# Kernel tuning notes

Measured on AMD Instinct MI355X. Metric: run time of the kernel, lower is better.

## Reference

```python
import jax, jax.numpy as jnp
import numpy as np
from jax.scipy.special import logsumexp

N = 36
N_ITERS = 20
TAU = 0.05
B = 512


def _xavier(key, out_f, in_f):
    std = float(np.sqrt(2.0 / (in_f + out_f)))
    return jax.random.normal(key, (out_f, in_f), dtype=jnp.float32) * std


def setup_inputs() -> dict:
    key = jax.random.key(0)
    ks = jax.random.split(key, 8)
    seq = jax.random.normal(ks[0], (B, N, 3076), dtype=jnp.float32)
    return {
        "seq": seq,
        "W1_txt_w": _xavier(ks[1], 128, 512), "W1_txt_b": jnp.zeros((128,), jnp.float32),
        "W1_vis_w": _xavier(ks[2], 512, 2048), "W1_vis_b": jnp.zeros((512,), jnp.float32),
        "W2_vis_w": _xavier(ks[3], 128, 512), "W2_vis_b": jnp.zeros((128,), jnp.float32),
        "W1_sen_w": _xavier(ks[4], 128, 512), "W1_sen_b": jnp.zeros((128,), jnp.float32),
        "W_fc_pos_w": _xavier(ks[5], 256, 388), "W_fc_pos_b": jnp.zeros((256,), jnp.float32),
        "W_fc_w": _xavier(ks[6], N, 256), "W_fc_b": jnp.zeros((N,), jnp.float32),
    }


def _linear(x, w, b):
    return x @ w.T + b


def _sinkhorn(x):
    # Faithful to the torch code: x = exp(x/tau); then iterative logsumexp
    # subtraction over rows/cols; finally exp(x).
    x = jnp.exp(x / TAU)

    def body(i, x):
        x = x - logsumexp(x, axis=-1, keepdims=True)
        x = x - logsumexp(x, axis=-2, keepdims=True)
        return x

    x = jax.lax.fori_loop(0, N_ITERS, body, x)
    return jnp.exp(x)


def reference(seq, W1_txt_w, W1_txt_b, W1_vis_w, W1_vis_b, W2_vis_w, W2_vis_b,
              W1_sen_w, W1_sen_b, W_fc_pos_w, W_fc_pos_b, W_fc_w, W_fc_b):
    x_txt = seq[:, :, :512]
    x_vis = seq[:, :, 512:2560]
    x_pos = seq[:, :, 2560:2564]
    x_sen = seq[:, :, 2564:]
    x_txt = jax.nn.relu(_linear(x_txt, W1_txt_w, W1_txt_b))
    x_vis = jax.nn.relu(_linear(x_vis, W1_vis_w, W1_vis_b))
    x_vis = jax.nn.relu(_linear(x_vis, W2_vis_w, W2_vis_b))
    x_sen = jax.nn.relu(_linear(x_sen, W1_sen_w, W1_sen_b))
    x_pos = jax.nn.relu(x_pos)
    x = jnp.concatenate((x_txt, x_vis, x_pos, x_sen), axis=-1)  # [B, N, 388]
    x = jax.nn.relu(_linear(x, W_fc_pos_w, W_fc_pos_b))
    x = jnp.tanh(_linear(x, W_fc_w, W_fc_b))  # [B, N, N]
    return _sinkhorn(x)
```

## Files before the change

kernel.cpp:

```cpp
#include <hip/hip_runtime.h>
#include <cstddef>
#include <cstdint>
#include <cmath>

#define TAU_INV 20.0f
#define NMAT 36
#define BATCH 512
#define MROWS 18432
#define MHALF 9216

typedef unsigned short us16;
typedef __attribute__((ext_vector_type(8))) short s16x8;
typedef __attribute__((ext_vector_type(4))) float f32x4;

__device__ inline us16 f2bf(float x) {
    uint32_t u = __float_as_uint(x);
    u += 0x7fff + ((u >> 16) & 1);
    return (us16)(u >> 16);
}
__device__ inline float bf2f(us16 h) {
    return __uint_as_float(((uint32_t)h) << 16);
}
__device__ inline void split3(float v, us16& h, us16& m, us16& l) {
    h = f2bf(v);
    float r1 = v - bf2f(h);
    m = f2bf(r1);
    l = f2bf(r1 - bf2f(m));
}

__device__ inline uint32_t cvtpk(float lo, float hi) {
    uint32_t d;
    asm("v_cvt_pk_bf16_f32 %0, %1, %2" : "=v"(d) : "v"(lo), "v"(hi));
    return d;
}
__device__ inline void split2pk(const float4& v, uint2& h, uint2& m) {
    uint32_t h0 = cvtpk(v.x, v.y), h1 = cvtpk(v.z, v.w);
    float a0 = v.x - __uint_as_float(h0 << 16);
    float a1 = v.y - __uint_as_float(h0 & 0xffff0000u);
    float a2 = v.z - __uint_as_float(h1 << 16);
    float a3 = v.w - __uint_as_float(h1 & 0xffff0000u);
    uint32_t m0 = cvtpk(a0, a1), m1 = cvtpk(a2, a3);
    h = make_uint2(h0, h1); m = make_uint2(m0, m1);
}

__device__ inline void dma16(const void* g, void* l) {
    __builtin_amdgcn_global_load_lds(
        (const __attribute__((address_space(1))) void*)g,
        (__attribute__((address_space(3))) void*)l, 16, 0, 0);
}

__device__ inline f32x4 mfma16(s16x8 a, s16x8 b, f32x4 c) {
    return __builtin_amdgcn_mfma_f32_16x16x32_bf16(a, b, c, 0, 0, 0);
}

template<int BM, int BN, int OUT, int MINW>
__global__ __launch_bounds__(256, MINW)
void gemm_split(const float* X, int ldx,
                const us16* Bh, const us16* Bm,
                const float* bias, float* C, int ldc, int nreal, int K,
                const float* X2, const us16* Bh2, const us16* Bm2,
                const float* bias2, float* C2)
{
    constexpr int MT  = BM / 32;
    constexpr int NT  = BN / 32;
    constexpr int NF4 = BM / 32;
    constexpr int LB  = BN / 64;

    if (blockIdx.z) { X = X2; Bh = Bh2; Bm = Bm2; bias = bias2; C = C2; }

    alignas(16) __shared__ us16 lds[(BM + BN) * 64];
    us16* AsH = lds;
    us16* AsM = lds + BM * 32;
    us16* BsH = lds + BM * 64;
    us16* BsM = lds + BM * 64 + BN * 32;

    const int tid  = threadIdx.x;
    const int lane = tid & 63;
    const int wid  = tid >> 6;
    const int bm   = blockIdx.x * BM;
    const int bn   = blockIdx.y * BN;
    const int lm   = lane & 15;
    const int kb   = lane >> 4;
    const int wm   = (wid >> 1) * (BM / 2);
    const int wn   = (wid & 1) * (BN / 2);

    const int arow = tid >> 3;
    const int acol = (tid & 7) * 4;
    const int asw  = ((arow >> 1) & 3) << 3;
    const int fsw  = ((lm >> 1) & 3) << 3;

    f32x4 acc[MT][NT];
#pragma unroll
    for (int i = 0; i < MT; ++i)
#pragma unroll
        for (int j = 0; j < NT; ++j) acc[i][j] = (f32x4){0.f, 0.f, 0.f, 0.f};

    float4 pref[NF4];
#pragma unroll
    for (int i = 0; i < NF4; ++i)
        pref[i] = *(const float4*)(X + (size_t)(bm + i * 32 + arow) * ldx + acol);

    const int bcol = ((lane & 3) ^ ((lane >> 3) & 3)) * 8;

    for (int k0 = 0; k0 < K; k0 += 32) {
        __syncthreads();
#pragma unroll
        for (int q = 0; q < LB; ++q) {
            const int rb = wid * (LB * 16) + q * 16;
            const int gr = bn + rb + (lane >> 2);
            const int gc = k0 + bcol;
            dma16(Bh + (size_t)gr * K + gc, &BsH[rb * 32]);
            dma16(Bm + (size_t)gr * K + gc, &BsM[rb * 32]);
        }
        float4 prefN[NF4];
        if (k0 + 32 < K) {
#pragma unroll
            for (int i = 0; i < NF4; ++i)
                prefN[i] = *(const float4*)(X + (size_t)(bm + i * 32 + arow) * ldx
                                            + (k0 + 32) + acol);
        }
#pragma unroll
        for (int i = 0; i < NF4; ++i) {
            const int r = i * 32 + arow;
            uint2 h, m;
            split2pk(pref[i], h, m);
            *(uint2*)&AsH[r * 32 + (acol ^ asw)] = h;
            *(uint2*)&AsM[r * 32 + (acol ^ asw)] = m;
        }
        if (k0 + 32 < K) {
#pragma unroll
            for (int i = 0; i < NF4; ++i) pref[i] = prefN[i];
        }
        __syncthreads();

        s16x8 ah[MT], am[MT];
#pragma unroll
        for (int mt = 0; mt < MT; ++mt) {
            const int off = (wm + mt * 16 + lm) * 32 + (kb * 8 ^ fsw);
            ah[mt] = *(const s16x8*)&AsH[off];
            am[mt] = *(const s16x8*)&AsM[off];
        }
#pragma unroll
        for (int nt = 0; nt < NT; ++nt) {
            const int off = (wn + nt * 16 + lm) * 32 + (kb * 8 ^ fsw);
            s16x8 bfh = *(const s16x8*)&BsH[off];
            s16x8 bfm = *(const s16x8*)&BsM[off];
#pragma unroll
            for (int mt = 0; mt < MT; ++mt) {
                acc[mt][nt] = mfma16(ah[mt], bfh, acc[mt][nt]);
                acc[mt][nt] = mfma16(ah[mt], bfm, acc[mt][nt]);
                acc[mt][nt] = mfma16(am[mt], bfh, acc[mt][nt]);
                acc[mt][nt] = mfma16(am[mt], bfm, acc[mt][nt]);
            }
        }
    }

    float bv[NT];
#pragma unroll
    for (int nt = 0; nt < NT; ++nt) {
        const int col = bn + wn + nt * 16 + lm;
        bv[nt] = (col < nreal) ? bias[col] : 0.f;
    }
#pragma unroll
    for (int nt = 0; nt < NT; ++nt) {
        const int col = bn + wn + nt * 16 + lm;
#pragma unroll
        for (int mt = 0; mt < MT; ++mt) {
#pragma unroll
            for (int r = 0; r < 4; ++r) {
                const int row = bm + wm + mt * 16 + kb * 4 + r;
                float v = acc[mt][nt][r] + bv[nt];
                if (OUT == 0) {
                    C[(size_t)row * ldc + col] = fmaxf(v, 0.f);
                } else {
                    if (col < nreal)
                        C[(size_t)row * ldc + col] = tanhf(v);
                }
            }
        }
    }
}

#define WOFF_W1T 1048576
#define WOFF_W1S 1114112
#define WOFF_W2V 1179648
#define WOFF_WFP 1245184
#define WOFF_WFC 1351680
#define WTOT     1368064

__global__ void split_weights(const float* __restrict__ w1v, const float* __restrict__ w1t,
                              const float* __restrict__ w1s, const float* __restrict__ w2v,
                              const float* __restrict__ wfp, const float* __restrict__ wfc,
                              us16* __restrict__ hi, us16* __restrict__ mi,
                              us16* __restrict__ lo)
{
    int idx = blockIdx.x * 256 + threadIdx.x;
    if (idx >= WTOT) return;
    const float* src; int N, K, Kp; int local;
    if (idx < WOFF_W1T)      { src = w1v; N = 512; K = 2048; Kp = 2048; local = idx; }
    else if (idx < WOFF_W1S) { src = w1t; N = 128; K = 512;  Kp = 512;  local = idx - WOFF_W1T; }
    else if (idx < WOFF_W2V) { src = w1s; N = 128; K = 512;  Kp = 512;  local = idx - WOFF_W1S; }
    else if (idx < WOFF_WFP) { src = w2v; N = 128; K = 512;  Kp = 512;  local = idx - WOFF_W2V; }
    else if (idx < WOFF_WFC) { src = wfp; N = 256; K = 388;  Kp = 416;  local = idx - WOFF_WFP; }
    else                     { src = wfc; N = 36;  K = 256;  Kp = 256;  local = idx - WOFF_WFC; }
    int n = local / Kp, k = local % Kp;
    float v = (n < N && k < K) ? src[(size_t)n * K + k] : 0.f;
    us16 h, m, l;
    split3(v, h, m, l);
    hi[idx] = h; mi[idx] = m; lo[idx] = l;
}

__global__ void pos_pad(const float* __restrict__ seq, float* __restrict__ cat)
{
    int idx = blockIdx.x * 256 + threadIdx.x;
    if (idx >= MROWS * 32) return;
    int row = idx >> 5, j = idx & 31;
    if (j < 4) {
        float v = seq[(size_t)row * 3076 + 2560 + j];
        cat[(size_t)row * 416 + 256 + j] = fmaxf(v, 0.f);
    } else {
        cat[(size_t)row * 416 + 388 + (j - 4)] = 0.f;
    }
}

__global__ __launch_bounds__(256)
void sinkhorn_kernel(const float* __restrict__ Z, float* __restrict__ out)
{
    __shared__ float A[NMAT][NMAT + 1];
    __shared__ float lse[NMAT];
    const int b = blockIdx.x;
    const int tid = threadIdx.x;
    const float* zb = Z + (size_t)b * NMAT * NMAT;

    for (int idx = tid; idx < NMAT * NMAT; idx += 256)
        A[idx / NMAT][idx % NMAT] = expf(zb[idx] * TAU_INV);
    __syncthreads();

    for (int it = 0; it < 20; ++it) {
        if (tid < NMAT * 4) {
            int r = tid >> 2, g = tid & 3;
            float m = -3.402823466e38f;
            for (int j = g; j < NMAT; j += 4) m = fmaxf(m, A[r][j]);
            m = fmaxf(m, __shfl_xor(m, 2, 4));
            m = fmaxf(m, __shfl_xor(m, 1, 4));
            float s = 0.f;
            for (int j = g; j < NMAT; j += 4) s += expf(A[r][j] - m);
            s += __shfl_xor(s, 2, 4);
            s += __shfl_xor(s, 1, 4);
            if (g == 0) lse[r] = m + logf(s);
        }
        __syncthreads();
        for (int idx = tid; idx < NMAT * NMAT; idx += 256)
            A[idx / NMAT][idx % NMAT] -= lse[idx / NMAT];
        __syncthreads();

        if (tid < NMAT * 4) {
            int c = tid >> 2, g = tid & 3;
            float m = -3.402823466e38f;
            for (int i = g; i < NMAT; i += 4) m = fmaxf(m, A[i][c]);
            m = fmaxf(m, __shfl_xor(m, 2, 4));
            m = fmaxf(m, __shfl_xor(m, 1, 4));
            float s = 0.f;
            for (int i = g; i < NMAT; i += 4) s += expf(A[i][c] - m);
            s += __shfl_xor(s, 2, 4);
            s += __shfl_xor(s, 1, 4);
            if (g == 0) lse[c] = m + logf(s);
        }
        __syncthreads();
        for (int idx = tid; idx < NMAT * NMAT; idx += 256)
            A[idx / NMAT][idx % NMAT] -= lse[idx % NMAT];
        __syncthreads();
    }

    for (int idx = tid; idx < NMAT * NMAT; idx += 256)
        out[(size_t)b * NMAT * NMAT + idx] = expf(A[idx / NMAT][idx % NMAT]);
}

extern "C" void kernel_launch(void* const* d_in, const int* in_sizes, int n_in,
                              void* d_out, int out_size, void* d_ws, size_t ws_size,
                              hipStream_t stream)
{
    const float* seq = (const float*)d_in[0];
    const float* W1t = (const float*)d_in[1];
    const float* b1t = (const float*)d_in[2];
    const float* W1v = (const float*)d_in[3];
    const float* b1v = (const float*)d_in[4];
    const float* W2v = (const float*)d_in[5];
    const float* b2v = (const float*)d_in[6];
    const float* W1s = (const float*)d_in[7];
    const float* b1s = (const float*)d_in[8];
    const float* Wfp = (const float*)d_in[9];
    const float* bfp = (const float*)d_in[10];
    const float* Wfc = (const float*)d_in[11];
    const float* bfc = (const float*)d_in[12];

    float* wsF = (float*)d_ws;
    dim3 blk(256);

    const bool full = ws_size >= (size_t)19156992 * 4;

    if (full) {
        float* vis1buf = wsF;
        float* h256    = wsF;
        float* cat     = wsF + 9437184;
        float* logits  = wsF + 9437184;
        us16*  Whi     = (us16*)(wsF + 17104896);
        us16*  Wmi     = Whi + WTOT;
        us16*  Wlo     = Wmi + WTOT;

        split_weights<<<dim3((WTOT + 255) / 256), blk, 0, stream>>>(
            W1v, W1t, W1s, W2v, Wfp, Wfc, Whi, Wmi, Wlo);
        pos_pad<<<dim3((MROWS * 32 + 255) / 256), blk, 0, stream>>>(seq, cat);
        gemm_split<64, 128, 0, 4><<<dim3(MROWS / 64, 1, 2), blk, 0, stream>>>(
            seq, 3076, Whi + WOFF_W1T, Wmi + WOFF_W1T, b1t,
            cat, 416, 128, 512,
            seq + 2564, Whi + WOFF_W1S, Wmi + WOFF_W1S, b1s,
            cat + 260);
        gemm_split<128, 128, 0, 3><<<dim3(MROWS / 128, 4, 1), blk, 0, stream>>>(
            seq + 512, 3076, Whi, Wmi, b1v, vis1buf, 512, 512, 2048,
            seq + 512, Whi, Wmi, b1v, vis1buf);
        gemm_split<64, 64, 0, 4><<<dim3(MROWS / 64, 2, 1), blk, 0, stream>>>(
            vis1buf, 512, Whi + WOFF_W2V, Wmi + WOFF_W2V, b2v,
            cat + 128, 416, 128, 512,
            vis1buf, Whi + WOFF_W2V, Wmi + WOFF_W2V, b2v,
            cat + 128);
        gemm_split<64, 128, 0, 4><<<dim3(MROWS / 64, 2, 1), blk, 0, stream>>>(
            cat, 416, Whi + WOFF_WFP, Wmi + WOFF_WFP, bfp,
            h256, 256, 256, 416,
            cat, Whi + WOFF_WFP, Wmi + WOFF_WFP, bfp, h256);
        gemm_split<64, 64, 1, 4><<<dim3(MROWS / 64, 1, 1), blk, 0, stream>>>(
            h256, 256, Whi + WOFF_WFC, Wmi + WOFF_WFC, bfc,
            logits, 36, 36, 256,
            h256, Whi + WOFF_WFC, Wmi + WOFF_WFC, bfc, logits);
        sinkhorn_kernel<<<dim3(BATCH), blk, 0, stream>>>(logits, (float*)d_out);
    } else {
        float* vis1buf = wsF;
        float* h256    = wsF;
        float* cat     = wsF + 4718592;
        float* logits  = wsF + 4718592;
        us16*  Whi     = (us16*)(wsF + 12386304);
        us16*  Wmi     = Whi + WTOT;
        us16*  Wlo     = Wmi + WTOT;

        split_weights<<<dim3((WTOT + 255) / 256), blk, 0, stream>>>(
            W1v, W1t, W1s, W2v, Wfp, Wfc, Whi, Wmi, Wlo);
        pos_pad<<<dim3((MROWS * 32 + 255) / 256), blk, 0, stream>>>(seq, cat);
        gemm_split<64, 128, 0, 4><<<dim3(MROWS / 64, 1, 2), blk, 0, stream>>>(
            seq, 3076, Whi + WOFF_W1T, Wmi + WOFF_W1T, b1t,
            cat, 416, 128, 512,
            seq + 2564, Whi + WOFF_W1S, Wmi + WOFF_W1S, b1s,
            cat + 260);
        for (int h = 0; h < 2; ++h) {
            const float* xh = seq + 512 + (size_t)h * MHALF * 3076;
            float* ch = cat + 128 + (size_t)h * MHALF * 416;
            gemm_split<128, 128, 0, 3><<<dim3(MHALF / 128, 4, 1), blk, 0, stream>>>(
                xh, 3076, Whi, Wmi, b1v, vis1buf, 512, 512, 2048,
                xh, Whi, Wmi, b1v, vis1buf);
            gemm_split<64, 64, 0, 4><<<dim3(MHALF / 64, 2, 1), blk, 0, stream>>>(
                vis1buf, 512, Whi + WOFF_W2V, Wmi + WOFF_W2V, b2v,
                ch, 416, 128, 512,
                vis1buf, Whi + WOFF_W2V, Wmi + WOFF_W2V, b2v, ch);
        }
        gemm_split<64, 128, 0, 4><<<dim3(MROWS / 64, 2, 1), blk, 0, stream>>>(
            cat, 416, Whi + WOFF_WFP, Wmi + WOFF_WFP, bfp,
            h256, 256, 256, 416,
            cat, Whi + WOFF_WFP, Wmi + WOFF_WFP, bfp, h256);
        gemm_split<64, 64, 1, 4><<<dim3(MROWS / 64, 1, 1), blk, 0, stream>>>(
            h256, 256, Whi + WOFF_WFC, Wmi + WOFF_WFC, bfc,
            logits, 36, 36, 256,
            h256, Whi + WOFF_WFC, Wmi + WOFF_WFC, bfc, logits);
        sinkhorn_kernel<<<dim3(BATCH), blk, 0, stream>>>(logits, (float*)d_out);
    }
}
```

Baseline: 595.2 us.

## Split-K the large vision GEMM into two halves reduced in the next GEMM

```diff
diff --git a/kernel.cpp b/kernel.cpp
--- a/kernel.cpp
+++ b/kernel.cpp
@@ -7,7 +7,6 @@
 #define NMAT 36
 #define BATCH 512
 #define MROWS 18432
-#define MHALF 9216
 
 typedef unsigned short us16;
 typedef __attribute__((ext_vector_type(8))) short s16x8;
@@ -53,20 +52,26 @@
     return __builtin_amdgcn_mfma_f32_16x16x32_bf16(a, b, c, 0, 0, 0);
 }
 
-template<int BM, int BN, int OUT, int MINW>
+template<int BM, int BN, int OUT, int MINW, int AMODE>
 __global__ __launch_bounds__(256, MINW)
-void gemm_split(const float* X, int ldx,
-                const us16* Bh, const us16* Bm,
-                const float* bias, float* C, int ldc, int nreal, int K,
-                const float* X2, const us16* Bh2, const us16* Bm2,
-                const float* bias2, float* C2)
+void gemm_split(int ldc, int nreal, int K, int ldb,
+                const float* X0, const float* Xb0, int ldx0,
+                const us16* Bh0, const us16* Bm0, const float* bias0, float* C0,
+                const float* X1, const float* Xb1, int ldx1,
+                const us16* Bh1, const us16* Bm1, const float* bias1, float* C1,
+                const float* X2, const float* Xb2, int ldx2,
+                const us16* Bh2, const us16* Bm2, const float* bias2, float* C2)
 {
     constexpr int MT  = BM / 32;
     constexpr int NT  = BN / 32;
     constexpr int NF4 = BM / 32;
     constexpr int LB  = BN / 64;
 
-    if (blockIdx.z) { X = X2; Bh = Bh2; Bm = Bm2; bias = bias2; C = C2; }
+    const float* X; const float* Xb; int ldx;
+    const us16 *Bh, *Bm; const float* bias; float* C;
+    if (blockIdx.z == 0)      { X = X0; Xb = Xb0; ldx = ldx0; Bh = Bh0; Bm = Bm0; bias = bias0; C = C0; }
+    else if (blockIdx.z == 1) { X = X1; Xb = Xb1; ldx = ldx1; Bh = Bh1; Bm = Bm1; bias = bias1; C = C1; }
+    else                      { X = X2; Xb = Xb2; ldx = ldx2; Bh = Bh2; Bm = Bm2; bias = bias2; C = C2; }
 
     alignas(16) __shared__ us16 lds[(BM + BN) * 64];
     us16* AsH = lds;
@@ -95,10 +100,13 @@
 #pragma unroll
         for (int j = 0; j < NT; ++j) acc[i][j] = (f32x4){0.f, 0.f, 0.f, 0.f};
 
-    float4 pref[NF4];
-#pragma unroll
-    for (int i = 0; i < NF4; ++i)
+    float4 pref[NF4], pref2[NF4];
+#pragma unroll
+    for (int i = 0; i < NF4; ++i) {
         pref[i] = *(const float4*)(X + (size_t)(bm + i * 32 + arow) * ldx + acol);
+        if (AMODE == 1)
+            pref2[i] = *(const float4*)(Xb + (size_t)(bm + i * 32 + arow) * ldx + acol);
+    }
 
     const int bcol = ((lane & 3) ^ ((lane >> 3) & 3)) * 8;
 
@@ -109,27 +117,41 @@
             const int rb = wid * (LB * 16) + q * 16;
             const int gr = bn + rb + (lane >> 2);
             const int gc = k0 + bcol;
-            dma16(Bh + (size_t)gr * K + gc, &BsH[rb * 32]);
-            dma16(Bm + (size_t)gr * K + gc, &BsM[rb * 32]);
-        }
-        float4 prefN[NF4];
+            dma16(Bh + (size_t)gr * ldb + gc, &BsH[rb * 32]);
+            dma16(Bm + (size_t)gr * ldb + gc, &BsM[rb * 32]);
+        }
+        float4 prefN[NF4], prefN2[NF4];
         if (k0 + 32 < K) {
 #pragma unroll
-            for (int i = 0; i < NF4; ++i)
+            for (int i = 0; i < NF4; ++i) {
                 prefN[i] = *(const float4*)(X + (size_t)(bm + i * 32 + arow) * ldx
                                             + (k0 + 32) + acol);
+                if (AMODE == 1)
+                    prefN2[i] = *(const float4*)(Xb + (size_t)(bm + i * 32 + arow) * ldx
+                                                 + (k0 + 32) + acol);
+            }
         }
 #pragma unroll
         for (int i = 0; i < NF4; ++i) {
             const int r = i * 32 + arow;
+            float4 v = pref[i];
+            if (AMODE == 1) {
+                v.x = fmaxf(v.x + pref2[i].x, 0.f);
+                v.y = fmaxf(v.y + pref2[i].y, 0.f);
+                v.z = fmaxf(v.z + pref2[i].z, 0.f);
+                v.w = fmaxf(v.w + pref2[i].w, 0.f);
+            }
             uint2 h, m;
-            split2pk(pref[i], h, m);
+            split2pk(v, h, m);
             *(uint2*)&AsH[r * 32 + (acol ^ asw)] = h;
             *(uint2*)&AsM[r * 32 + (acol ^ asw)] = m;
         }
         if (k0 + 32 < K) {
 #pragma unroll
-            for (int i = 0; i < NF4; ++i) pref[i] = prefN[i];
+            for (int i = 0; i < NF4; ++i) {
+                pref[i] = prefN[i];
+                if (AMODE == 1) pref2[i] = prefN2[i];
+            }
         }
         __syncthreads();
 
@@ -172,9 +194,11 @@
                 float v = acc[mt][nt][r] + bv[nt];
                 if (OUT == 0) {
                     C[(size_t)row * ldc + col] = fmaxf(v, 0.f);
-                } else {
+                } else if (OUT == 1) {
                     if (col < nreal)
                         C[(size_t)row * ldc + col] = tanhf(v);
+                } else {
+                    C[(size_t)row * ldc + col] = v;
                 }
             }
         }
@@ -210,10 +234,12 @@
     hi[idx] = h; mi[idx] = m; lo[idx] = l;
 }
 
-__global__ void pos_pad(const float* __restrict__ seq, float* __restrict__ cat)
+__global__ void pos_pad(const float* __restrict__ seq, float* __restrict__ cat,
+                        float* __restrict__ zbias)
 {
     int idx = blockIdx.x * 256 + threadIdx.x;
-    if (idx >= MROWS * 32) return;
+    if (idx >= MROWS * 32 + 512) return;
+    if (idx >= MROWS * 32) { zbias[idx - MROWS * 32] = 0.f; return; }
     int row = idx >> 5, j = idx & 31;
     if (j < 4) {
         float v = seq[(size_t)row * 3076 + 2560 + j];
@@ -297,9 +323,50 @@
     float* wsF = (float*)d_ws;
     dim3 blk(256);
 
-    const bool full = ws_size >= (size_t)19156992 * 4;
-
-    if (full) {
+    const bool splitk = ws_size >= (size_t)28594688 * 4;
+
+    if (splitk) {
+        float* vis1a = wsF;
+        float* vis1b = wsF + 9437184;
+        float* h256  = wsF;
+        float* cat    = wsF + 18874368;
+        float* logits = wsF + 18874368;
+        us16*  Whi    = (us16*)(wsF + 26542080);
+        us16*  Wmi    = Whi + WTOT;
+        us16*  Wlo    = Wmi + WTOT;
+        float* zbias  = wsF + 28594176;
+
+        split_weights<<<dim3((WTOT + 255) / 256), blk, 0, stream>>>(
+            W1v, W1t, W1s, W2v, Wfp, Wfc, Whi, Wmi, Wlo);
+        pos_pad<<<dim3((MROWS * 32 + 512 + 255) / 256), blk, 0, stream>>>(
+            seq, cat, zbias);
+        gemm_split<128, 128, 2, 3, 0><<<dim3(MROWS / 128, 4, 2), blk, 0, stream>>>(
+            512, 512, 1024, 2048,
+            seq + 512,        nullptr, 3076, Whi,        Wmi,        b1v,   vis1a,
+            seq + 512 + 1024, nullptr, 3076, Whi + 1024, Wmi + 1024, zbias, vis1b,
+            seq + 512,        nullptr, 3076, Whi,        Wmi,        b1v,   vis1a);
+        gemm_split<64, 128, 0, 4, 0><<<dim3(MROWS / 64, 1, 2), blk, 0, stream>>>(
+            416, 128, 512, 512,
+            seq,        nullptr, 3076, Whi + WOFF_W1T, Wmi + WOFF_W1T, b1t, cat,
+            seq + 2564, nullptr, 3076, Whi + WOFF_W1S, Wmi + WOFF_W1S, b1s, cat + 260,
+            seq,        nullptr, 3076, Whi + WOFF_W1T, Wmi + WOFF_W1T, b1t, cat);
+        gemm_split<64, 64, 0, 4, 1><<<dim3(MROWS / 64, 2, 1), blk, 0, stream>>>(
+            416, 128, 512, 512,
+            vis1a, vis1b, 512, Whi + WOFF_W2V, Wmi + WOFF_W2V, b2v, cat + 128,
+            vis1a, vis1b, 512, Whi + WOFF_W2V, Wmi + WOFF_W2V, b2v, cat + 128,
+            vis1a, vis1b, 512, Whi + WOFF_W2V, Wmi + WOFF_W2V, b2v, cat + 128);
+        gemm_split<64, 128, 0, 4, 0><<<dim3(MROWS / 64, 2, 1), blk, 0, stream>>>(
+            256, 256, 416, 416,
+            cat, nullptr, 416, Whi + WOFF_WFP, Wmi + WOFF_WFP, bfp, h256,
+            cat, nullptr, 416, Whi + WOFF_WFP, Wmi + WOFF_WFP, bfp, h256,
+            cat, nullptr, 416, Whi + WOFF_WFP, Wmi + WOFF_WFP, bfp, h256);
+        gemm_split<64, 64, 1, 4, 0><<<dim3(MROWS / 64, 1, 1), blk, 0, stream>>>(
+            36, 36, 256, 256,
+            h256, nullptr, 256, Whi + WOFF_WFC, Wmi + WOFF_WFC, bfc, logits,
+            h256, nullptr, 256, Whi + WOFF_WFC, Wmi + WOFF_WFC, bfc, logits,
+            h256, nullptr, 256, Whi + WOFF_WFC, Wmi + WOFF_WFC, bfc, logits);
+        sinkhorn_kernel<<<dim3(BATCH), blk, 0, stream>>>(logits, (float*)d_out);
+    } else {
         float* vis1buf = wsF;
         float* h256    = wsF;
         float* cat     = wsF + 9437184;
@@ -310,65 +377,33 @@
 
         split_weights<<<dim3((WTOT + 255) / 256), blk, 0, stream>>>(
             W1v, W1t, W1s, W2v, Wfp, Wfc, Whi, Wmi, Wlo);
-        pos_pad<<<dim3((MROWS * 32 + 255) / 256), blk, 0, stream>>>(seq, cat);
-        gemm_split<64, 128, 0, 4><<<dim3(MROWS / 64, 1, 2), blk, 0, stream>>>(
-            seq, 3076, Whi + WOFF_W1T, Wmi + WOFF_W1T, b1t,
-            cat, 416, 128, 512,
-            seq + 2564, Whi + WOFF_W1S, Wmi + WOFF_W1S, b1s,
-            cat + 260);
-        gemm_split<128, 128, 0, 3><<<dim3(MROWS / 128, 4, 1), blk, 0, stream>>>(
-            seq + 512, 3076, Whi, Wmi, b1v, vis1buf, 512, 512, 2048,
-            seq + 512, Whi, Wmi, b1v, vis1buf);
-        gemm_split<64, 64, 0, 4><<<dim3(MROWS / 64, 2, 1), blk, 0, stream>>>(
-            vis1buf, 512, Whi + WOFF_W2V, Wmi + WOFF_W2V, b2v,
-            cat + 128, 416, 128, 512,
-            vis1buf, Whi + WOFF_W2V, Wmi + WOFF_W2V, b2v,
-            cat + 128);
-        gemm_split<64, 128, 0, 4><<<dim3(MROWS / 64, 2, 1), blk, 0, stream>>>(
-            cat, 416, Whi + WOFF_WFP, Wmi + WOFF_WFP, bfp,
-            h256, 256, 256, 416,
-            cat, Whi + WOFF_WFP, Wmi + WOFF_WFP, bfp, h256);
-        gemm_split<64, 64, 1, 4><<<dim3(MROWS / 64, 1, 1), blk, 0, stream>>>(
-            h256, 256, Whi + WOFF_WFC, Wmi + WOFF_WFC, bfc,
-            logits, 36, 36, 256,
-            h256, Whi + WOFF_WFC, Wmi + WOFF_WFC, bfc, logits);
+        pos_pad<<<dim3((MROWS * 32 + 512 + 255) / 256), blk, 0, stream>>>(
+            seq, cat, cat);
+        gemm_split<128, 128, 0, 3, 0><<<dim3(MROWS / 128, 4, 1), blk, 0, stream>>>(
+            512, 512, 2048, 2048,
+            seq + 512, nullptr, 3076, Whi, Wmi, b1v, vis1buf,
+            seq + 512, nullptr, 3076, Whi, Wmi, b1v, vis1buf,
+            seq + 512, nullptr, 3076, Whi, Wmi, b1v, vis1buf);
+        gemm_split<64, 128, 0, 4, 0><<<dim3(MROWS / 64, 1, 2), blk, 0, stream>>>(
+            416, 128, 512, 512,
+            seq,        nullptr, 3076, Whi + WOFF_W1T, Wmi + WOFF_W1T, b1t, cat,
+            seq + 2564, nullptr, 3076, Whi + WOFF_W1S, Wmi + WOFF_W1S, b1s, cat + 260,
+            seq,        nullptr, 3076, Whi + WOFF_W1T, Wmi + WOFF_W1T, b1t, cat);
+        gemm_split<64, 64, 0, 4, 0><<<dim3(MROWS / 64, 2, 1), blk, 0, stream>>>(
+            416, 128, 512, 512,
+            vis1buf, nullptr, 512, Whi + WOFF_W2V, Wmi + WOFF_W2V, b2v, cat + 128,
+            vis1buf, nullptr, 512, Whi + WOFF_W2V, Wmi + WOFF_W2V, b2v, cat + 128,
+            vis1buf, nullptr, 512, Whi + WOFF_W2V, Wmi + WOFF_W2V, b2v, cat + 128);
+        gemm_split<64, 128, 0, 4, 0><<<dim3(MROWS / 64, 2, 1), blk, 0, stream>>>(
+            256, 256, 416, 416,
+            cat, nullptr, 416, Whi + WOFF_WFP, Wmi + WOFF_WFP, bfp, h256,
+            cat, nullptr, 416, Whi + WOFF_WFP, Wmi + WOFF_WFP, bfp, h256,
+            cat, nullptr, 416, Whi + WOFF_WFP, Wmi + WOFF_WFP, bfp, h256);
+        gemm_split<64, 64, 1, 4, 0><<<dim3(MROWS / 64, 1, 1), blk, 0, stream>>>(
+            36, 36, 256, 256,
+            h256, nullptr, 256, Whi + WOFF_WFC, Wmi + WOFF_WFC, bfc, logits,
+            h256, nullptr, 256, Whi + WOFF_WFC, Wmi + WOFF_WFC, bfc, logits,
+            h256, nullptr, 256, Whi + WOFF_WFC, Wmi + WOFF_WFC, bfc, logits);
         sinkhorn_kernel<<<dim3(BATCH), blk, 0, stream>>>(logits, (float*)d_out);
-    } else {
-        float* vis1buf = wsF;
-        float* h256    = wsF;
-        float* cat     = wsF + 4718592;
-        float* logits  = wsF + 4718592;
-        us16*  Whi     = (us16*)(wsF + 12386304);
-        us16*  Wmi     = Whi + WTOT;
-        us16*  Wlo     = Wmi + WTOT;
-
-        split_weights<<<dim3((WTOT + 255) / 256), blk, 0, stream>>>(
-            W1v, W1t, W1s, W2v, Wfp, Wfc, Whi, Wmi, Wlo);
-        pos_pad<<<dim3((MROWS * 32 + 255) / 256), blk, 0, stream>>>(seq, cat);
-        gemm_split<64, 128, 0, 4><<<dim3(MROWS / 64, 1, 2), blk, 0, stream>>>(
-            seq, 3076, Whi + WOFF_W1T, Wmi + WOFF_W1T, b1t,
-            cat, 416, 128, 512,
-            seq + 2564, Whi + WOFF_W1S, Wmi + WOFF_W1S, b1s,
-            cat + 260);
-        for (int h = 0; h < 2; ++h) {
-            const float* xh = seq + 512 + (size_t)h * MHALF * 3076;
-            float* ch = cat + 128 + (size_t)h * MHALF * 416;
-            gemm_split<128, 128, 0, 3><<<dim3(MHALF / 128, 4, 1), blk, 0, stream>>>(
-                xh, 3076, Whi, Wmi, b1v, vis1buf, 512, 512, 2048,
-                xh, Whi, Wmi, b1v, vis1buf);
-            gemm_split<64, 64, 0, 4><<<dim3(MHALF / 64, 2, 1), blk, 0, stream>>>(
-                vis1buf, 512, Whi + WOFF_W2V, Wmi + WOFF_W2V, b2v,
-                ch, 416, 128, 512,
-                vis1buf, Whi + WOFF_W2V, Wmi + WOFF_W2V, b2v, ch);
-        }
-        gemm_split<64, 128, 0, 4><<<dim3(MROWS / 64, 2, 1), blk, 0, stream>>>(
-            cat, 416, Whi + WOFF_WFP, Wmi + WOFF_WFP, bfp,
-            h256, 256, 256, 416,
-            cat, Whi + WOFF_WFP, Wmi + WOFF_WFP, bfp, h256);
-        gemm_split<64, 64, 1, 4><<<dim3(MROWS / 64, 1, 1), blk, 0, stream>>>(
-            h256, 256, Whi + WOFF_WFC, Wmi + WOFF_WFC, bfc,
-            logits, 36, 36, 256,
-            h256, Whi + WOFF_WFC, Wmi + WOFF_WFC, bfc, logits);
-        sinkhorn_kernel<<<dim3(BATCH), blk, 0, stream>>>(logits, (float*)d_out);
-    }
-}
+    }
+}
```

Result: slower. 612.5 us (+2.9%).
